# Performance work log

Hardware: AMD Instinct MI355X
Metric: run time of the kernel (lower is better)

The kernel has to match this reference:

```python
import math
import jax, jax.numpy as jnp
import numpy as np

B, T, C, H = 4, 2048, 1024, 16
D = C // H          # head dim 64
FF = 4 * C          # 4096

def setup_inputs() -> dict:
    key = jax.random.key(0)
    ks = jax.random.split(key, 7)
    s = 0.02
    return {
        "x":      jax.random.normal(ks[0], (B, T, C), jnp.float32),
        "g1":     jnp.ones((C,), jnp.float32),                      # ln_1 weight (bias=False)
        "w_qkv":  jax.random.normal(ks[1], (3 * C, C), jnp.float32) * s,  # torch Linear [out,in]
        "w_o":    jax.random.normal(ks[2], (C, C), jnp.float32) * s,
        "g2":     jnp.ones((C,), jnp.float32),                      # ln_2 weight
        "w_fc":   jax.random.normal(ks[3], (FF, C), jnp.float32) * s,
        "w_proj": jax.random.normal(ks[4], (C, FF), jnp.float32) * s,
    }

def _layernorm(x, g):
    mu = jnp.mean(x, axis=-1, keepdims=True)
    var = jnp.mean(jnp.square(x - mu), axis=-1, keepdims=True)
    return (x - mu) * jax.lax.rsqrt(var + 1e-5) * g

def _attn(x, w_qkv, w_o):
    qkv = x @ w_qkv.T                                  # [B,T,3C]
    q, k, v = jnp.split(qkv, 3, axis=-1)
    q = q.reshape(B, T, H, D).transpose(0, 2, 1, 3)    # [B,H,T,D]
    k = k.reshape(B, T, H, D).transpose(0, 2, 1, 3)
    v = v.reshape(B, T, H, D).transpose(0, 2, 1, 3)
    att = jnp.einsum('bhtd,bhsd->bhts', q, k) * (1.0 / math.sqrt(D))
    mask = jnp.tril(jnp.ones((T, T), bool))
    att = jnp.where(mask, att, -jnp.inf)
    att = jax.nn.softmax(att, axis=-1)
    y = jnp.einsum('bhts,bhsd->bhtd', att, v)          # [B,H,T,D]
    y = y.transpose(0, 2, 1, 3).reshape(B, T, C)
    return y @ w_o.T

def _mlp(x, w_fc, w_proj):
    h = jax.nn.gelu(x @ w_fc.T, approximate=False)     # torch nn.GELU default = exact erf
    return h @ w_proj.T

def reference(x, g1, w_qkv, w_o, g2, w_fc, w_proj):
    x = x + _attn(_layernorm(x, g1), w_qkv, w_o)
    x = x + _mlp(_layernorm(x, g2), w_fc, w_proj)
    return x
```

## Files before the change

kernel.cpp:

```cpp
#include <hip/hip_runtime.h>

typedef __attribute__((ext_vector_type(8))) short bs8;
typedef __attribute__((ext_vector_type(4))) short bs4;
typedef __attribute__((ext_vector_type(4))) float f32x4;

__device__ __forceinline__ float b2f(short u) {
  union { unsigned int i; float f; } c;
  c.i = ((unsigned int)(unsigned short)u) << 16;
  return c.f;
}
__device__ __forceinline__ unsigned short f2bs(float f) {
  union { float f; unsigned int i; } c; c.f = f;
  unsigned int r = (c.i + 0x7FFFu + ((c.i >> 16) & 1u)) >> 16;
  return (unsigned short)r;
}
__device__ __forceinline__ void async16(const void* g, void* l) {
  __builtin_amdgcn_global_load_lds((__attribute__((address_space(1))) void*)g,
                                   (__attribute__((address_space(3))) void*)l, 16, 0, 0);
}

__device__ __forceinline__ float gelu_fast(float v) {
  const float x = v * 0.70710678118654752f;
  const float ax = fabsf(x);
  const float t = 1.0f / (1.0f + 0.3275911f * ax);
  float p = 1.061405429f;
  p = p * t - 1.453152027f;
  p = p * t + 1.421413741f;
  p = p * t - 0.284496736f;
  p = p * t + 0.254829592f;
  const float e = __expf(-ax * ax);
  float er = 1.0f - p * t * e;
  er = copysignf(er, x);
  return 0.5f * v * (1.0f + er);
}

__global__ __launch_bounds__(256) void cvt_ln_kernel(const void* __restrict__ xsrc,
                                                     const void* __restrict__ g1src,
                                                     unsigned short* __restrict__ xc,
                                                     unsigned short* __restrict__ xn) {
  const int row = blockIdx.x;
  const int tid = threadIdx.x;
  const int isf32 = (((const unsigned int*)g1src)[0] == 0x3F800000u) ? 1 : 0;
  const size_t base = (size_t)row * 1024 + tid * 4;
  float v[4], g[4];
  if (isf32) {
    const float4 t = *(const float4*)((const float*)xsrc + base);
    v[0] = t.x; v[1] = t.y; v[2] = t.z; v[3] = t.w;
    const float4 gt = *(const float4*)((const float*)g1src + tid * 4);
    g[0] = gt.x; g[1] = gt.y; g[2] = gt.z; g[3] = gt.w;
  } else {
    const bs4 t = *(const bs4*)((const unsigned short*)xsrc + base);
    v[0] = b2f(t[0]); v[1] = b2f(t[1]); v[2] = b2f(t[2]); v[3] = b2f(t[3]);
    const bs4 gt = *(const bs4*)((const unsigned short*)g1src + tid * 4);
    g[0] = b2f(gt[0]); g[1] = b2f(gt[1]); g[2] = b2f(gt[2]); g[3] = b2f(gt[3]);
  }
  { bs4 o; o[0] = f2bs(v[0]); o[1] = f2bs(v[1]); o[2] = f2bs(v[2]); o[3] = f2bs(v[3]);
    *(bs4*)(xc + base) = o; }
  float s  = v[0] + v[1] + v[2] + v[3];
  float sq = v[0]*v[0] + v[1]*v[1] + v[2]*v[2] + v[3]*v[3];
  for (int off = 32; off > 0; off >>= 1) { s += __shfl_xor(s, off); sq += __shfl_xor(sq, off); }
  __shared__ float sm[8];
  const int wv = tid >> 6;
  if ((tid & 63) == 0) { sm[wv] = s; sm[4 + wv] = sq; }
  __syncthreads();
  s  = sm[0] + sm[1] + sm[2] + sm[3];
  sq = sm[4] + sm[5] + sm[6] + sm[7];
  const float mu = s * (1.0f / 1024.0f);
  const float rstd = rsqrtf(sq * (1.0f / 1024.0f) - mu * mu + 1e-5f);
  unsigned short* op = xn + base;
  #pragma unroll
  for (int i = 0; i < 4; ++i) op[i] = f2bs((v[i] - mu) * rstd * g[i]);
}

struct CvtArgs {
  const void* src[5];
  unsigned short* dst[5];
  int start[6];
};
__global__ __launch_bounds__(256) void cvt_all_kernel(CvtArgs a,
                                                      const unsigned int* __restrict__ g1raw) {
  const int isf32 = (g1raw[0] == 0x3F800000u) ? 1 : 0;
  int blk = blockIdx.x;
  int seg = 0;
  #pragma unroll
  for (int s = 1; s < 5; ++s) if (blk >= a.start[s]) seg = s;
  const int i = ((blk - a.start[seg]) * 256 + threadIdx.x) * 4;
  const void* src = a.src[seg];
  unsigned short* dst = a.dst[seg];
  if (isf32) {
    const float4 t = *(const float4*)((const float*)src + i);
    bs4 o; o[0] = f2bs(t.x); o[1] = f2bs(t.y); o[2] = f2bs(t.z); o[3] = f2bs(t.w);
    *(bs4*)(dst + i) = o;
  } else {
    *(bs4*)(dst + i) = *(const bs4*)((const unsigned short*)src + i);
  }
}

__global__ __launch_bounds__(256) void ln_kernel(const unsigned short* __restrict__ xin,
                                                 const unsigned short* __restrict__ g,
                                                 unsigned short* __restrict__ out) {
  const int row = blockIdx.x;
  const int tid = threadIdx.x;
  const size_t base = (size_t)row * 1024 + tid * 4;
  float v[4];
  const bs4 t = *(const bs4*)(xin + base);
  v[0] = b2f(t[0]); v[1] = b2f(t[1]); v[2] = b2f(t[2]); v[3] = b2f(t[3]);
  float s  = v[0] + v[1] + v[2] + v[3];
  float sq = v[0]*v[0] + v[1]*v[1] + v[2]*v[2] + v[3]*v[3];
  for (int off = 32; off > 0; off >>= 1) { s += __shfl_xor(s, off); sq += __shfl_xor(sq, off); }
  __shared__ float sm[8];
  const int wv = tid >> 6;
  if ((tid & 63) == 0) { sm[wv] = s; sm[4 + wv] = sq; }
  __syncthreads();
  s  = sm[0] + sm[1] + sm[2] + sm[3];
  sq = sm[4] + sm[5] + sm[6] + sm[7];
  const float mu = s * (1.0f / 1024.0f);
  const float rstd = rsqrtf(sq * (1.0f / 1024.0f) - mu * mu + 1e-5f);
  const bs4 gt = *(const bs4*)(g + tid * 4);
  unsigned short* op = out + base;
  #pragma unroll
  for (int i = 0; i < 4; ++i) op[i] = f2bs((v[i] - mu) * rstd * b2f(gt[i]));
}

template<int EPI, int NBN>
__global__ __launch_bounds__(256, 2) void gemm_bt(const unsigned short* __restrict__ X,
                                                  const unsigned short* __restrict__ W,
                                                  const unsigned short* __restrict__ res,
                                                  void* __restrict__ out,
                                                  const unsigned int* __restrict__ g1raw,
                                                  int M, int N, int K) {
  __shared__ __align__(16) unsigned short Alds[2][128 * 64];
  __shared__ __align__(16) unsigned short Blds[2][128 * 64];
  const int tid  = threadIdx.x;
  const int wave = tid >> 6, lane = tid & 63;
  const int c16 = lane & 15, q8 = (lane >> 4) * 8;
  const int wm = (wave >> 1) * 64, wn = (wave & 1) * 64;

  const int nbn = gridDim.x;
  const int d = blockIdx.y * nbn + blockIdx.x;
  const int xcd = d & 7, slot = d >> 3;
  const int cpx = (nbn * gridDim.y) >> 3;
  const int sq = xcd * (cpx >> 6) + (slot >> 6);
  const int r  = slot & 63;
  const int nsx = nbn >> 3;
  const int bn0 = ((sq % nsx) * 8 + (r & 7)) * 128;
  const int bm  = ((sq / nsx) * 8 + (r >> 3)) * 128;
  const int bstride = N / NBN;

  const int sw = (c16 & 7) << 4;

  int isf32 = 0;
  if constexpr (EPI == 3) isf32 = (g1raw[0] == 0x3F800000u) ? 1 : 0;

  f32x4 acc[4][4] = {};

  const int srow = tid >> 3;
  const int scb  = ((tid & 7) * 16) ^ ((srow & 7) << 4);

  auto STAGE = [&](int j, int k0, int b) {
    const int bnj = bn0 + j * bstride;
    #pragma unroll
    for (int it = 0; it < 4; ++it) {
      const int row = it * 32 + srow;
      async16((const char*)X + ((size_t)(bm + row) * K + k0) * 2 + scb,
              (char*)&Alds[b][0] + (it * 256 + tid) * 16);
      async16((const char*)W + ((size_t)(bnj + row) * K + k0) * 2 + scb,
              (char*)&Blds[b][0] + (it * 256 + tid) * 16);
    }
  };

  auto COMPUTE = [&](int b) {
    const char* Ab = (const char*)&Alds[b][0];
    const char* Bb = (const char*)&Blds[b][0];
    #pragma unroll
    for (int kk = 0; kk < 64; kk += 32) {
      bs8 af[4], bf[4];
      #pragma unroll
      for (int mi = 0; mi < 4; ++mi)
        af[mi] = *(const bs8*)(Ab + (wm + mi * 16 + c16) * 128 + (((kk + q8) * 2) ^ sw));
      #pragma unroll
      for (int ni = 0; ni < 4; ++ni)
        bf[ni] = *(const bs8*)(Bb + (wn + ni * 16 + c16) * 128 + (((kk + q8) * 2) ^ sw));
      #pragma unroll
      for (int mi = 0; mi < 4; ++mi)
        #pragma unroll
        for (int ni = 0; ni < 4; ++ni)
          acc[mi][ni] = __builtin_amdgcn_mfma_f32_16x16x32_bf16(af[mi], bf[ni], acc[mi][ni], 0, 0, 0);
    }
  };

  const int q4 = (lane >> 4) * 4;

  STAGE(0, 0, 0);
  int cur = 0;
  for (int j = 0; j < NBN; ++j) {
    for (int k0 = 0; k0 < K; k0 += 64) {
      const bool last = (j == NBN - 1) && (k0 == K - 64);
      if (!last) {
        int nj = j, nk = k0 + 64;
        if (nk == K) { nj = j + 1; nk = 0; }
        STAGE(nj, nk, cur ^ 1);
        asm volatile("s_waitcnt vmcnt(8)" ::: "memory");
      } else {
        asm volatile("s_waitcnt vmcnt(0)" ::: "memory");
      }
      __builtin_amdgcn_s_barrier();
      COMPUTE(cur);
      __builtin_amdgcn_s_barrier();
      cur ^= 1;
    }

    const int bnj = bn0 + j * bstride;
    #pragma unroll
    for (int mi = 0; mi < 4; ++mi) {
      #pragma unroll
      for (int r2 = 0; r2 < 4; ++r2) {
        const size_t row = bm + wm + mi * 16 + q4 + r2;
        #pragma unroll
        for (int ni = 0; ni < 4; ++ni) {
          const size_t col = bnj + wn + ni * 16 + c16;
          const size_t idx = row * (size_t)N + col;
          float v = acc[mi][ni][r2];
          if constexpr (EPI == 0) {
            ((unsigned short*)out)[idx] = f2bs(v);
          } else if constexpr (EPI == 1) {
            ((unsigned short*)out)[idx] = f2bs(gelu_fast(v));
          } else if constexpr (EPI == 2) {
            v += b2f(res[idx]);
            ((unsigned short*)out)[idx] = f2bs(v);
          } else {
            v += b2f(res[idx]);
            if (isf32) ((float*)out)[idx] = v;
            else       ((unsigned short*)out)[idx] = f2bs(v);
          }
          acc[mi][ni][r2] = 0.0f;
        }
      }
    }
  }
}

__global__ __launch_bounds__(256) void vtrans_kernel(const unsigned short* __restrict__ qkv,
                                                     unsigned short* __restrict__ vt) {
  constexpr int T = 2048, C3 = 3072;
  __shared__ __align__(16) unsigned short tile[64][72];
  const int tid = threadIdx.x;
  const int t0 = blockIdx.x * 64;
  const int bh = blockIdx.y; const int b = bh >> 4, h = bh & 15;
  const int r = tid >> 3, c = (tid & 7) * 8;
  #pragma unroll
  for (int it = 0; it < 2; ++it) {
    const int t = it * 32 + r;
    *(bs8*)&tile[t][c] = *(const bs8*)(qkv + ((size_t)(b * T + t0 + t)) * C3 + 2048 + h * 64 + c);
  }
  __syncthreads();
  #pragma unroll
  for (int it = 0; it < 2; ++it) {
    const int d = it * 32 + r;
    bs8 o;
    #pragma unroll
    for (int j = 0; j < 8; ++j) o[j] = (short)tile[c + j][d];
    *(bs8*)(vt + ((size_t)bh * 64 + d) * T + t0 + c) = o;
  }
}

struct KF { bs8 a[4][2]; };

__device__ __forceinline__ void ldsFrag(KF& f, const char* buf, int c16, int quad) {
  const int sw = (c16 & 7) << 4;
  #pragma unroll
  for (int g = 0; g < 4; ++g) {
    const int rowb = (g * 16 + c16) * 128 + quad * 16;
    f.a[g][0] = *(const bs8*)(buf + ((rowb) ^ sw));
    f.a[g][1] = *(const bs8*)(buf + ((rowb + 64) ^ sw));
  }
}

template<bool DO_A, bool MA, bool MB>
__device__ __forceinline__ void tile2(const char* Kb, const char* Vb, int kvbase,
                                      const bs8& qfA0, const bs8& qfA1,
                                      const bs8& qfB0, const bs8& qfB1,
                                      f32x4 (&oA)[4], f32x4 (&oB)[4],
                                      float (&lsA)[4], float (&lsB)[4],
                                      char* Pw, int qrowA, int qrowB,
                                      int c16, int quad) {
  KF kf, vf;
  ldsFrag(kf, Kb, c16, quad);
  ldsFrag(vf, Vb, c16, quad);

  f32x4 sA[4], sB[4];
  __builtin_amdgcn_s_setprio(1);
  #pragma unroll
  for (int g = 0; g < 4; ++g) {
    if constexpr (DO_A) {
      f32x4 z = {};
      z = __builtin_amdgcn_mfma_f32_16x16x32_bf16(qfA0, kf.a[g][0], z, 0, 0, 0);
      sA[g] = __builtin_amdgcn_mfma_f32_16x16x32_bf16(qfA1, kf.a[g][1], z, 0, 0, 0);
    }
    f32x4 z2 = {};
    z2 = __builtin_amdgcn_mfma_f32_16x16x32_bf16(qfB0, kf.a[g][0], z2, 0, 0, 0);
    sB[g] = __builtin_amdgcn_mfma_f32_16x16x32_bf16(qfB1, kf.a[g][1], z2, 0, 0, 0);
  }
  __builtin_amdgcn_s_setprio(0);

  #pragma unroll
  for (int r = 0; r < 4; ++r) {
    const int prow = quad * 4 + r;
    const int pbase = prow * 128;
    const int psw = (prow & 7) << 4;
    #pragma unroll
    for (int g = 0; g < 4; ++g) {
      const int col2 = (g * 16 + c16) * 2;
      if constexpr (DO_A) {
        float p = __expf(sA[g][r] * 0.125f - 4.0f);
        if constexpr (MA) { if (kvbase + g * 16 + c16 > qrowA + r) p = 0.f; }
        lsA[r] += p;
        *(unsigned short*)(Pw + ((pbase + col2) ^ psw)) = f2bs(p);
      }
      float p2 = __expf(sB[g][r] * 0.125f - 4.0f);
      if constexpr (MB) { if (kvbase + g * 16 + c16 > qrowB + r) p2 = 0.f; }
      lsB[r] += p2;
      *(unsigned short*)(Pw + 2048 + ((pbase + col2) ^ psw)) = f2bs(p2);
    }
  }
  asm volatile("s_waitcnt lgkmcnt(0)" ::: "memory");

  const int rsw = (c16 & 7) << 4;
  const int rbase = c16 * 128 + quad * 16;
  bs8 pA0, pA1;
  if constexpr (DO_A) {
    pA0 = *(const bs8*)(Pw + ((rbase) ^ rsw));
    pA1 = *(const bs8*)(Pw + ((rbase + 64) ^ rsw));
  }
  const bs8 pB0 = *(const bs8*)(Pw + 2048 + ((rbase) ^ rsw));
  const bs8 pB1 = *(const bs8*)(Pw + 2048 + ((rbase + 64) ^ rsw));
  __builtin_amdgcn_s_setprio(1);
  #pragma unroll
  for (int g = 0; g < 4; ++g) {
    if constexpr (DO_A) {
      oA[g] = __builtin_amdgcn_mfma_f32_16x16x32_bf16(pA0, vf.a[g][0], oA[g], 0, 0, 0);
      oA[g] = __builtin_amdgcn_mfma_f32_16x16x32_bf16(pA1, vf.a[g][1], oA[g], 0, 0, 0);
    }
    oB[g] = __builtin_amdgcn_mfma_f32_16x16x32_bf16(pB0, vf.a[g][0], oB[g], 0, 0, 0);
    oB[g] = __builtin_amdgcn_mfma_f32_16x16x32_bf16(pB1, vf.a[g][1], oB[g], 0, 0, 0);
  }
  __builtin_amdgcn_s_setprio(0);
}

__global__ __launch_bounds__(256) void attn_kernel(const unsigned short* __restrict__ qkv,
                                                   const unsigned short* __restrict__ vt,
                                                   unsigned short* __restrict__ y) {
  constexpr int T = 2048, C3 = 3072, CC = 1024;
  __shared__ __align__(16) unsigned short Klds[2][4096];
  __shared__ __align__(16) unsigned short Vlds[2][4096];
  __shared__ __align__(16) unsigned short Plds[4][2048];

  const int tid = threadIdx.x;
  const int wv = tid >> 6, lane = tid & 63;
  const int quad = lane >> 4, c16 = lane & 15;
  const int bh = blockIdx.x;
  const int b = bh >> 4, h = bh & 15;
  const int i = blockIdx.y;
  const int qA = i, qB = 31 - i;
  const size_t rowbase = (size_t)b * T;
  char* Pw = (char*)&Plds[wv][0];

  const int y0 = tid * 16, y1 = 4096 + tid * 16;
  const int r0 = y0 >> 7, r1 = y1 >> 7;
  const int s0 = y0 ^ ((r0 & 7) << 4);
  const int s1 = y1 ^ ((r1 & 7) << 4);
  const char* Ksrc0 = (const char*)qkv + ((size_t)(b * T) + r0) * 6144 + 2048 + h * 128 + (s0 & 127);
  const char* Ksrc1 = (const char*)qkv + ((size_t)(b * T) + r1) * 6144 + 2048 + h * 128 + (s1 & 127);
  const char* Vsrc0 = (const char*)vt + ((size_t)bh * 64 + r0) * (T * 2) + (s0 & 127);
  const char* Vsrc1 = (const char*)vt + ((size_t)bh * 64 + r1) * (T * 2) + (s1 & 127);

  auto STAGE = [&](int kt, int buf) {
    char* Kb = (char*)&Klds[buf][0];
    char* Vb = (char*)&Vlds[buf][0];
    const size_t ko = (size_t)kt * (64 * 6144);
    const int vo = kt * 128;
    async16(Ksrc0 + ko, Kb + y0);
    async16(Ksrc1 + ko, Kb + y1);
    async16(Vsrc0 + vo, Vb + y0);
    async16(Vsrc1 + vo, Vb + y1);
  };

  STAGE(0, 0);

  bs8 qfA0, qfA1, qfB0, qfB1;
  {
    const unsigned short* qpA = qkv + (rowbase + qA * 64 + wv * 16 + c16) * C3 + h * 64 + quad * 8;
    qfA0 = *(const bs8*)qpA; qfA1 = *(const bs8*)(qpA + 32);
    const unsigned short* qpB = qkv + (rowbase + qB * 64 + wv * 16 + c16) * C3 + h * 64 + quad * 8;
    qfB0 = *(const bs8*)qpB; qfB1 = *(const bs8*)(qpB + 32);
  }
  const int qrowA = qA * 64 + wv * 16 + quad * 4;
  const int qrowB = qB * 64 + wv * 16 + quad * 4;

  f32x4 oA[4] = {}, oB[4] = {};
  float lsA[4] = {}, lsB[4] = {};

  __syncthreads();

  int cur = 0, kt = 0;
  for (; kt < qA; ++kt) {
    STAGE(kt + 1, cur ^ 1);
    tile2<true, false, false>((const char*)&Klds[cur][0], (const char*)&Vlds[cur][0], kt * 64,
                              qfA0, qfA1, qfB0, qfB1, oA, oB, lsA, lsB, Pw, qrowA, qrowB, c16, quad);
    __syncthreads(); cur ^= 1;
  }
  STAGE(kt + 1, cur ^ 1);
  tile2<true, true, false>((const char*)&Klds[cur][0], (const char*)&Vlds[cur][0], kt * 64,
                           qfA0, qfA1, qfB0, qfB1, oA, oB, lsA, lsB, Pw, qrowA, qrowB, c16, quad);
  __syncthreads(); cur ^= 1; ++kt;
  for (; kt < qB; ++kt) {
    STAGE(kt + 1, cur ^ 1);
    tile2<false, false, false>((const char*)&Klds[cur][0], (const char*)&Vlds[cur][0], kt * 64,
                               qfA0, qfA1, qfB0, qfB1, oA, oB, lsA, lsB, Pw, qrowA, qrowB, c16, quad);
    __syncthreads(); cur ^= 1;
  }
  tile2<false, false, true>((const char*)&Klds[cur][0], (const char*)&Vlds[cur][0], kt * 64,
                            qfA0, qfA1, qfB0, qfB1, oA, oB, lsA, lsB, Pw, qrowA, qrowB, c16, quad);

  #pragma unroll
  for (int r = 0; r < 4; ++r) {
    for (int off = 1; off < 16; off <<= 1) {
      lsA[r] += __shfl_xor(lsA[r], off);
      lsB[r] += __shfl_xor(lsB[r], off);
    }
  }

  #pragma unroll
  for (int r = 0; r < 4; ++r) {
    const float invA = 1.0f / lsA[r];
    unsigned short* ypA = y + (rowbase + qrowA + r) * CC + h * 64 + c16;
    ypA[0]  = f2bs(oA[0][r] * invA);
    ypA[16] = f2bs(oA[1][r] * invA);
    ypA[32] = f2bs(oA[2][r] * invA);
    ypA[48] = f2bs(oA[3][r] * invA);
    const float invB = 1.0f / lsB[r];
    unsigned short* ypB = y + (rowbase + qrowB + r) * CC + h * 64 + c16;
    ypB[0]  = f2bs(oB[0][r] * invB);
    ypB[16] = f2bs(oB[1][r] * invB);
    ypB[32] = f2bs(oB[2][r] * invB);
    ypB[48] = f2bs(oB[3][r] * invB);
  }
}

extern "C" void kernel_launch(void* const* d_in, const int* in_sizes, int n_in,
                              void* d_out, int out_size, void* d_ws, size_t ws_size,
                              hipStream_t stream) {
  char* ws = (char*)d_ws;
  unsigned short* xc     = (unsigned short*)(ws);
  unsigned short* wqkvc  = (unsigned short*)(ws + 16777216);
  unsigned short* woc    = (unsigned short*)(ws + 23068672);
  unsigned short* wfcc   = (unsigned short*)(ws + 25165824);
  unsigned short* wprojc = (unsigned short*)(ws + 33554432);
  unsigned short* g2c    = (unsigned short*)(ws + 41945088);
  unsigned short* vt     = (unsigned short*)(ws + 41947136);
  unsigned short* x1     = (unsigned short*)(ws + 41947136);
  unsigned short* qkv    = (unsigned short*)(ws + 58724352);
  unsigned short* hb     = (unsigned short*)(ws + 58724352);
  unsigned short* xn     = (unsigned short*)(ws + 125833216);
  unsigned short* yb     = (unsigned short*)(ws + 125833216);

  const int M = 8192;
  const unsigned int* g1raw = (const unsigned int*)d_in[1];

  cvt_ln_kernel<<<8192, 256, 0, stream>>>(d_in[0], d_in[1], xc, xn);

  CvtArgs ca;
  ca.src[0] = d_in[2]; ca.dst[0] = wqkvc;  int b0 = 3072;
  ca.src[1] = d_in[3]; ca.dst[1] = woc;    int b1 = 1024;
  ca.src[2] = d_in[4]; ca.dst[2] = g2c;    int b2 = 1;
  ca.src[3] = d_in[5]; ca.dst[3] = wfcc;   int b3 = 4096;
  ca.src[4] = d_in[6]; ca.dst[4] = wprojc; int b4 = 4096;
  ca.start[0] = 0;
  ca.start[1] = b0;
  ca.start[2] = b0 + b1;
  ca.start[3] = b0 + b1 + b2;
  ca.start[4] = b0 + b1 + b2 + b3;
  ca.start[5] = b0 + b1 + b2 + b3 + b4;
  cvt_all_kernel<<<ca.start[5], 256, 0, stream>>>(ca, g1raw);

  gemm_bt<0, 3><<<dim3(8, 64), 256, 0, stream>>>(xn, wqkvc, nullptr, qkv, nullptr, M, 3072, 1024);
  vtrans_kernel<<<dim3(32, 64), 256, 0, stream>>>(qkv, vt);
  attn_kernel<<<dim3(64, 16), 256, 0, stream>>>(qkv, vt, yb);
  gemm_bt<2, 1><<<dim3(8, 64), 256, 0, stream>>>(yb, woc, xc, x1, nullptr, M, 1024, 1024);
  ln_kernel<<<M, 256, 0, stream>>>(x1, g2c, xn);
  gemm_bt<1, 4><<<dim3(8, 64), 256, 0, stream>>>(xn, wfcc, nullptr, hb, nullptr, M, 4096, 1024);
  gemm_bt<3, 1><<<dim3(8, 64), 256, 0, stream>>>(hb, wprojc, x1, d_out, g1raw, M, 1024, 4096);
}
```

Baseline: 498.7 us.

## Replace double-buffered persistent GEMM with single-buffer one-tile-per-block GEMM

```diff
diff --git a/kernel.cpp b/kernel.cpp
--- a/kernel.cpp
+++ b/kernel.cpp
@@ -122,15 +122,15 @@
   for (int i = 0; i < 4; ++i) op[i] = f2bs((v[i] - mu) * rstd * b2f(gt[i]));
 }
 
-template<int EPI, int NBN>
-__global__ __launch_bounds__(256, 2) void gemm_bt(const unsigned short* __restrict__ X,
+template<int EPI>
+__global__ __launch_bounds__(256, 4) void gemm_bt(const unsigned short* __restrict__ X,
                                                   const unsigned short* __restrict__ W,
                                                   const unsigned short* __restrict__ res,
                                                   void* __restrict__ out,
                                                   const unsigned int* __restrict__ g1raw,
                                                   int M, int N, int K) {
-  __shared__ __align__(16) unsigned short Alds[2][128 * 64];
-  __shared__ __align__(16) unsigned short Blds[2][128 * 64];
+  __shared__ __align__(16) unsigned short Alds[128 * 64];
+  __shared__ __align__(16) unsigned short Blds[128 * 64];
   const int tid  = threadIdx.x;
   const int wave = tid >> 6, lane = tid & 63;
   const int c16 = lane & 15, q8 = (lane >> 4) * 8;
@@ -143,9 +143,8 @@
   const int sq = xcd * (cpx >> 6) + (slot >> 6);
   const int r  = slot & 63;
   const int nsx = nbn >> 3;
-  const int bn0 = ((sq % nsx) * 8 + (r & 7)) * 128;
-  const int bm  = ((sq / nsx) * 8 + (r >> 3)) * 128;
-  const int bstride = N / NBN;
+  const int bn = ((sq % nsx) * 8 + (r & 7)) * 128;
+  const int bm = ((sq / nsx) * 8 + (r >> 3)) * 128;
 
   const int sw = (c16 & 7) << 4;
 
@@ -157,21 +156,19 @@
   const int srow = tid >> 3;
   const int scb  = ((tid & 7) * 16) ^ ((srow & 7) << 4);
 
-  auto STAGE = [&](int j, int k0, int b) {
-    const int bnj = bn0 + j * bstride;
+  for (int k0 = 0; k0 < K; k0 += 64) {
     #pragma unroll
     for (int it = 0; it < 4; ++it) {
       const int row = it * 32 + srow;
       async16((const char*)X + ((size_t)(bm + row) * K + k0) * 2 + scb,
-              (char*)&Alds[b][0] + (it * 256 + tid) * 16);
-      async16((const char*)W + ((size_t)(bnj + row) * K + k0) * 2 + scb,
-              (char*)&Blds[b][0] + (it * 256 + tid) * 16);
-    }
-  };
-
-  auto COMPUTE = [&](int b) {
-    const char* Ab = (const char*)&Alds[b][0];
-    const char* Bb = (const char*)&Blds[b][0];
+              (char*)&Alds[0] + (it * 256 + tid) * 16);
+      async16((const char*)W + ((size_t)(bn + row) * K + k0) * 2 + scb,
+              (char*)&Blds[0] + (it * 256 + tid) * 16);
+    }
+    __syncthreads();
+
+    const char* Ab = (const char*)&Alds[0];
+    const char* Bb = (const char*)&Blds[0];
     #pragma unroll
     for (int kk = 0; kk < 64; kk += 32) {
       bs8 af[4], bf[4];
@@ -187,53 +184,31 @@
         for (int ni = 0; ni < 4; ++ni)
           acc[mi][ni] = __builtin_amdgcn_mfma_f32_16x16x32_bf16(af[mi], bf[ni], acc[mi][ni], 0, 0, 0);
     }
-  };
+    __syncthreads();
+  }
 
   const int q4 = (lane >> 4) * 4;
-
-  STAGE(0, 0, 0);
-  int cur = 0;
-  for (int j = 0; j < NBN; ++j) {
-    for (int k0 = 0; k0 < K; k0 += 64) {
-      const bool last = (j == NBN - 1) && (k0 == K - 64);
-      if (!last) {
-        int nj = j, nk = k0 + 64;
-        if (nk == K) { nj = j + 1; nk = 0; }
-        STAGE(nj, nk, cur ^ 1);
-        asm volatile("s_waitcnt vmcnt(8)" ::: "memory");
-      } else {
-        asm volatile("s_waitcnt vmcnt(0)" ::: "memory");
-      }
-      __builtin_amdgcn_s_barrier();
-      COMPUTE(cur);
-      __builtin_amdgcn_s_barrier();
-      cur ^= 1;
-    }
-
-    const int bnj = bn0 + j * bstride;
+  #pragma unroll
+  for (int mi = 0; mi < 4; ++mi) {
     #pragma unroll
-    for (int mi = 0; mi < 4; ++mi) {
+    for (int r2 = 0; r2 < 4; ++r2) {
+      const size_t row = bm + wm + mi * 16 + q4 + r2;
       #pragma unroll
-      for (int r2 = 0; r2 < 4; ++r2) {
-        const size_t row = bm + wm + mi * 16 + q4 + r2;
-        #pragma unroll
-        for (int ni = 0; ni < 4; ++ni) {
-          const size_t col = bnj + wn + ni * 16 + c16;
-          const size_t idx = row * (size_t)N + col;
-          float v = acc[mi][ni][r2];
-          if constexpr (EPI == 0) {
-            ((unsigned short*)out)[idx] = f2bs(v);
-          } else if constexpr (EPI == 1) {
-            ((unsigned short*)out)[idx] = f2bs(gelu_fast(v));
-          } else if constexpr (EPI == 2) {
-            v += b2f(res[idx]);
-            ((unsigned short*)out)[idx] = f2bs(v);
-          } else {
-            v += b2f(res[idx]);
-            if (isf32) ((float*)out)[idx] = v;
-            else       ((unsigned short*)out)[idx] = f2bs(v);
-          }
-          acc[mi][ni][r2] = 0.0f;
+      for (int ni = 0; ni < 4; ++ni) {
+        const size_t col = bn + wn + ni * 16 + c16;
+        const size_t idx = row * (size_t)N + col;
+        float v = acc[mi][ni][r2];
+        if constexpr (EPI == 0) {
+          ((unsigned short*)out)[idx] = f2bs(v);
+        } else if constexpr (EPI == 1) {
+          ((unsigned short*)out)[idx] = f2bs(gelu_fast(v));
+        } else if constexpr (EPI == 2) {
+          v += b2f(res[idx]);
+          ((unsigned short*)out)[idx] = f2bs(v);
+        } else {
+          v += b2f(res[idx]);
+          if (isf32) ((float*)out)[idx] = v;
+          else       ((unsigned short*)out)[idx] = f2bs(v);
         }
       }
     }
@@ -483,11 +458,11 @@
   ca.start[5] = b0 + b1 + b2 + b3 + b4;
   cvt_all_kernel<<<ca.start[5], 256, 0, stream>>>(ca, g1raw);
 
-  gemm_bt<0, 3><<<dim3(8, 64), 256, 0, stream>>>(xn, wqkvc, nullptr, qkv, nullptr, M, 3072, 1024);
+  gemm_bt<0><<<dim3(24, 64), 256, 0, stream>>>(xn, wqkvc, nullptr, qkv, nullptr, M, 3072, 1024);
   vtrans_kernel<<<dim3(32, 64), 256, 0, stream>>>(qkv, vt);
   attn_kernel<<<dim3(64, 16), 256, 0, stream>>>(qkv, vt, yb);
-  gemm_bt<2, 1><<<dim3(8, 64), 256, 0, stream>>>(yb, woc, xc, x1, nullptr, M, 1024, 1024);
+  gemm_bt<2><<<dim3(8, 64), 256, 0, stream>>>(yb, woc, xc, x1, nullptr, M, 1024, 1024);
   ln_kernel<<<M, 256, 0, stream>>>(x1, g2c, xn);
-  gemm_bt<1, 4><<<dim3(8, 64), 256, 0, stream>>>(xn, wfcc, nullptr, hb, nullptr, M, 4096, 1024);
-  gemm_bt<3, 1><<<dim3(8, 64), 256, 0, stream>>>(hb, wprojc, x1, d_out, g1raw, M, 1024, 4096);
-}
+  gemm_bt<1><<<dim3(32, 64), 256, 0, stream>>>(xn, wfcc, nullptr, hb, nullptr, M, 4096, 1024);
+  gemm_bt<3><<<dim3(8, 64), 256, 0, stream>>>(hb, wprojc, x1, d_out, g1raw, M, 1024, 4096);
+}
```

Result: faster. 461.0 us (-7.6%).
